# Optimization experiments

Hardware: AMD Instinct MI355X
Metric: run time of the kernel (lower is better)

The kernel has to match this reference:

```python
import jax, jax.numpy as jnp
import numpy as np

N_POINTS = 1 << 20
N_LEVELS = 16
F_PER_LVL = 2
LOG2_T = 19
T = 1 << LOG2_T
BASE_RES = 16
PER_LEVEL_SCALE = float(np.exp2(np.log2(2048.0 / 16.0) / (N_LEVELS - 1)))
# 8 trilinear corner offsets [8,3]
OFFSETS = np.stack(np.meshgrid(*([np.array([0, 1])] * 3), indexing='ij'), axis=-1).reshape(8, 3)
PRIMES = np.array([1, 2654435761, 805459861], dtype=np.uint32)  # tcnn spatial hash primes


def _level_params(l):
    # tcnn: grid_scale = 2^(l*log2(s)) * base - 1 ; resolution = ceil(scale)+1
    scale = np.exp2(l * np.log2(PER_LEVEL_SCALE)) * BASE_RES - 1.0
    res = int(np.ceil(scale)) + 1
    return float(scale), res


def hash_encode(x, table):
    """x: [N,3] in [0,1]; table: [L,T,F]. Returns [N, L*F]."""
    offs = jnp.asarray(OFFSETS)                     # [8,3] int32
    primes = jnp.asarray(PRIMES)                    # [3] uint32
    feats = []
    for l in range(N_LEVELS):
        scale, res = _level_params(l)
        pos = x * scale + 0.5                       # [N,3]
        pos_grid = jnp.floor(pos)
        w = pos - pos_grid                          # [N,3] interp weights
        c0 = pos_grid.astype(jnp.int32)             # [N,3]
        corners = c0[None, :, :] + offs[:, None, :]  # [8,N,3]
        if res ** 3 <= T:
            # dense indexing for coarse levels (fits in hashmap)
            cc = jnp.clip(corners, 0, res - 1)
            idx = cc[..., 0] + cc[..., 1] * res + cc[..., 2] * (res * res)
        else:
            cu = corners.astype(jnp.uint32)
            h = (cu[..., 0] * primes[0]) ^ (cu[..., 1] * primes[1]) ^ (cu[..., 2] * primes[2])
            idx = (h & jnp.uint32(T - 1)).astype(jnp.int32)
        f = table[l][idx]                           # [8,N,F] gather
        # trilinear weights: prod over dims of (w if corner bit else 1-w)
        wc = jnp.prod(jnp.where(offs[:, None, :] == 1, w[None], 1.0 - w[None]), axis=-1)  # [8,N]
        feats.append(jnp.sum(wc[..., None] * f, axis=0))  # [N,F]
    return jnp.concatenate(feats, axis=-1)          # [N, 32]


def _softplus10(z):
    return jax.nn.softplus(10.0 * z) / 10.0


def setup_inputs() -> dict:
    key = jax.random.key(0)
    k = jax.random.split(key, 6)
    x = jax.random.uniform(k[0], (N_POINTS, 3), dtype=jnp.float32)
    table = jax.random.normal(k[1], (N_LEVELS, T, F_PER_LVL), dtype=jnp.float32) * 1e-2
    w1 = jax.random.normal(k[2], (64, 32), dtype=jnp.float32) * 0.1
    w2 = jax.random.normal(k[3], (64, 64), dtype=jnp.float32) * 0.1
    w3 = jax.random.normal(k[4], (64, 64), dtype=jnp.float32) * 0.1
    w4 = jax.random.normal(k[5], (1, 64), dtype=jnp.float32) * 0.1
    return {"x": x, "table": table, "w1": w1, "w2": w2, "w3": w3, "w4": w4}


def reference(x, table, w1, w2, w3, w4):
    enc = hash_encode(x, table)                     # [N,32]
    h = _softplus10(enc @ w1.T)
    h = _softplus10(h @ w2.T)
    h = _softplus10(h @ w3.T)
    sdf = h @ w4.T                                  # [N,1]
    return sdf
```

## Files before the change

### kernel.cpp

```cpp
#include <hip/hip_runtime.h>
#include <cmath>

#define T_SIZE (1u << 19)

typedef _Float16 h8 __attribute__((ext_vector_type(8)));
typedef _Float16 h4 __attribute__((ext_vector_type(4)));
typedef _Float16 h2 __attribute__((ext_vector_type(2)));
typedef float f4 __attribute__((ext_vector_type(4)));

struct Levels {
    float scale[16];
    int   res[16];
    unsigned dense_mask;
};

__device__ __forceinline__ float softplus10(float z) {
    float e = __builtin_amdgcn_exp2f(fminf(z * 14.426950408889634f, 126.0f));
    return __builtin_amdgcn_logf(1.0f + e) * 0.069314718055994531f;
}

__global__ __launch_bounds__(256) void convert_table_kernel(
    const float2* __restrict__ t, h2* __restrict__ o, int total4)
{
    int i = blockIdx.x * 256 + threadIdx.x;
    if (i >= total4) return;
    const float2* src = t + (size_t)i * 4;
    h8 r;
#pragma unroll
    for (int j = 0; j < 4; ++j) {
        float2 v = src[j];
        r[2 * j]     = (_Float16)v.x;
        r[2 * j + 1] = (_Float16)v.y;
    }
    *(h8*)(o + (size_t)i * 4) = r;
}

__global__ __launch_bounds__(256) void convert_weights_kernel(
    const float* __restrict__ w1, const float* __restrict__ w2,
    const float* __restrict__ w3, _Float16* __restrict__ o)
{
    int i = blockIdx.x * 256 + threadIdx.x;
    float v;
    if (i < 2048)      v = w1[i];
    else if (i < 6144) v = w2[i - 2048];
    else               v = w3[i - 6144];
    o[i] = (_Float16)v;
}

__device__ __forceinline__ void gather_pair(
    const h2* __restrict__ tl, unsigned i0, unsigned i1,
    float2& v0, float2& v1)
{
    unsigned g = i0 & ~3u;
    union { h8 v; uint4 u; } cv;
    cv.v = *(const h8*)(tl + g);
    unsigned p0 = i0 & 3u;
    unsigned a01 = (p0 & 1u) ? cv.u.y : cv.u.x;
    unsigned a23 = (p0 & 1u) ? cv.u.w : cv.u.z;
    unsigned e0  = (p0 & 2u) ? a23 : a01;
    unsigned e1;
    if ((i1 & ~3u) == g) {
        unsigned p1 = i1 & 3u;
        unsigned b01 = (p1 & 1u) ? cv.u.y : cv.u.x;
        unsigned b23 = (p1 & 1u) ? cv.u.w : cv.u.z;
        e1 = (p1 & 2u) ? b23 : b01;
    } else {
        e1 = *(const unsigned*)(tl + i1);
    }
    h2 c0 = __builtin_bit_cast(h2, e0);
    h2 c1 = __builtin_bit_cast(h2, e1);
    v0 = make_float2((float)c0[0], (float)c0[1]);
    v1 = make_float2((float)c1[0], (float)c1[1]);
}

__global__ __launch_bounds__(256) void encode_kernel(
    const float* __restrict__ xs, const h2* __restrict__ table,
    h2* __restrict__ enc2, Levels lv, int lbase, int N)
{
    __shared__ float sx[768];
    __shared__ float s_scale[16];
    __shared__ int   s_res[16];

    const int i0 = blockIdx.x * 256;
    for (int t = threadIdx.x; t < 768; t += 256) sx[t] = xs[(size_t)i0 * 3 + t];
    if (threadIdx.x < 16) {
        s_scale[threadIdx.x] = lv.scale[threadIdx.x];
        s_res[threadIdx.x]   = lv.res[threadIdx.x];
    }
    __syncthreads();

    const int l = lbase + blockIdx.y;
    const int i = i0 + threadIdx.x;
    if (i >= N) return;

    const float px = sx[threadIdx.x * 3 + 0];
    const float py = sx[threadIdx.x * 3 + 1];
    const float pz = sx[threadIdx.x * 3 + 2];
    const float s  = s_scale[l];
    const int  res = s_res[l];

    float fx = px * s + 0.5f, fy = py * s + 0.5f, fz = pz * s + 0.5f;
    float gx = floorf(fx), gy = floorf(fy), gz = floorf(fz);
    float wx = fx - gx, wy = fy - gy, wz = fz - gz;
    int cx = (int)gx, cy = (int)gy, cz = (int)gz;

    const h2* tl = table + (size_t)l * T_SIZE;
    float2 vx0[4], vx1[4];

    if ((lv.dense_mask >> l) & 1u) {
        int r1 = res - 1;
        int x0 = min(cx, r1), x1 = min(cx + 1, r1);
        int y0 = min(cy, r1), y1 = min(cy + 1, r1);
        int z0 = min(cz, r1), z1 = min(cz + 1, r1);
        int rr = res * res;
        int bases[4] = {y0 * res + z0 * rr, y0 * res + z1 * rr,
                        y1 * res + z0 * rr, y1 * res + z1 * rr};
#pragma unroll
        for (int j = 0; j < 4; ++j)
            gather_pair(tl, (unsigned)(x0 + bases[j]), (unsigned)(x1 + bases[j]),
                        vx0[j], vx1[j]);
    } else {
        unsigned hy0 = (unsigned)cy * 2654435761u, hy1 = (unsigned)(cy + 1) * 2654435761u;
        unsigned hz0 = (unsigned)cz * 805459861u,  hz1 = (unsigned)(cz + 1) * 805459861u;
        unsigned Y[4] = {hy0 ^ hz0, hy0 ^ hz1, hy1 ^ hz0, hy1 ^ hz1};
        const unsigned M = T_SIZE - 1;
#pragma unroll
        for (int j = 0; j < 4; ++j)
            gather_pair(tl, ((unsigned)cx ^ Y[j]) & M,
                        ((unsigned)(cx + 1) ^ Y[j]) & M, vx0[j], vx1[j]);
    }

    float wx0 = 1.f - wx, wy0 = 1.f - wy, wz0 = 1.f - wz;
    float wyz[4] = {wy0 * wz0, wy0 * wz, wy * wz0, wy * wz};
    float f0 = 0.f, f1 = 0.f;
#pragma unroll
    for (int j = 0; j < 4; ++j) {
        float w0 = wx0 * wyz[j], w1 = wx * wyz[j];
        f0 += w0 * vx0[j].x + w1 * vx1[j].x;
        f1 += w0 * vx0[j].y + w1 * vx1[j].y;
    }

    h2 r;
    r[0] = (_Float16)f0;
    r[1] = (_Float16)f1;
    enc2[(size_t)l * N + i] = r;
}

template <typename WT>
__device__ __forceinline__ h8 load_frag8(const WT* p) {
    if constexpr (sizeof(WT) == 2) {
        return *(const h8*)p;
    } else {
        h8 r;
#pragma unroll
        for (int j = 0; j < 8; ++j) r[j] = (_Float16)p[j];
        return r;
    }
}

template <typename WT>
__global__ __launch_bounds__(256, 3) void mlp_kernel(
    const h2* __restrict__ enc2,
    const WT* __restrict__ w1, const WT* __restrict__ w2,
    const WT* __restrict__ w3, const float* __restrict__ w4,
    float* __restrict__ out, int nTiles, int N)
{
    constexpr int AR = 72;
    __shared__ __align__(16) _Float16 sAct[256 * AR];

    const int tid = threadIdx.x;
    const int wave = tid >> 6;
    const int lane = tid & 63;
    const int lrow = lane & 15;
    const int quad = lane >> 4;
    const int waveRow = wave * 64;
    const f4 zero = {0.f, 0.f, 0.f, 0.f};

    h8 aW1[4];
#pragma unroll
    for (int tm = 0; tm < 4; ++tm)
        aW1[tm] = load_frag8(w1 + (tm * 16 + lrow) * 32 + quad * 8);
    h8 aW2[4][2], aW3[4][2];
#pragma unroll
    for (int tm = 0; tm < 4; ++tm)
#pragma unroll
        for (int km = 0; km < 2; ++km) {
            aW2[tm][km] = load_frag8(w2 + (tm * 16 + lrow) * 64 + km * 32 + quad * 8);
            aW3[tm][km] = load_frag8(w3 + (tm * 16 + lrow) * 64 + km * 32 + quad * 8);
        }
    float w4f[16];
#pragma unroll
    for (int tm = 0; tm < 4; ++tm)
#pragma unroll
        for (int r = 0; r < 4; ++r)
            w4f[tm * 4 + r] = w4[tm * 16 + quad * 4 + r];

    for (int tile = blockIdx.x; tile < nTiles; tile += gridDim.x) {
        const int blockPt = tile * 256;

#pragma unroll
        for (int t = 0; t < 4; ++t) {
            const int ptg = blockPt + waveRow + t * 16 + lrow;
            h8 b;
#pragma unroll
            for (int d = 0; d < 4; ++d) {
                h2 p = enc2[(size_t)(quad * 4 + d) * N + ptg];
                b[2 * d]     = p[0];
                b[2 * d + 1] = p[1];
            }
            const int arow = (waveRow + t * 16 + lrow) * AR;
#pragma unroll
            for (int tm = 0; tm < 4; ++tm) {
                f4 acc = __builtin_amdgcn_mfma_f32_16x16x32_f16(aW1[tm], b, zero, 0, 0, 0);
                h4 pk;
#pragma unroll
                for (int r = 0; r < 4; ++r) pk[r] = (_Float16)softplus10(acc[r]);
                *(h4*)&sAct[arow + tm * 16 + quad * 4] = pk;
            }
        }

#pragma unroll
        for (int t = 0; t < 4; ++t) {
            const int arow = (waveRow + t * 16 + lrow) * AR;
            h8 b0 = *(const h8*)&sAct[arow + quad * 8];
            h8 b1 = *(const h8*)&sAct[arow + 32 + quad * 8];
            f4 accs[4];
#pragma unroll
            for (int tm = 0; tm < 4; ++tm) {
                f4 acc = __builtin_amdgcn_mfma_f32_16x16x32_f16(aW2[tm][0], b0, zero, 0, 0, 0);
                acc     = __builtin_amdgcn_mfma_f32_16x16x32_f16(aW2[tm][1], b1, acc,  0, 0, 0);
                accs[tm] = acc;
            }
#pragma unroll
            for (int tm = 0; tm < 4; ++tm) {
                h4 pk;
#pragma unroll
                for (int r = 0; r < 4; ++r) pk[r] = (_Float16)softplus10(accs[tm][r]);
                *(h4*)&sAct[arow + tm * 16 + quad * 4] = pk;
            }
        }

#pragma unroll
        for (int t = 0; t < 4; ++t) {
            const int arow = (waveRow + t * 16 + lrow) * AR;
            h8 b0 = *(const h8*)&sAct[arow + quad * 8];
            h8 b1 = *(const h8*)&sAct[arow + 32 + quad * 8];
            float sum = 0.f;
#pragma unroll
            for (int tm = 0; tm < 4; ++tm) {
                f4 acc = __builtin_amdgcn_mfma_f32_16x16x32_f16(aW3[tm][0], b0, zero, 0, 0, 0);
                acc     = __builtin_amdgcn_mfma_f32_16x16x32_f16(aW3[tm][1], b1, acc,  0, 0, 0);
#pragma unroll
                for (int r = 0; r < 4; ++r)
                    sum += w4f[tm * 4 + r] * softplus10(acc[r]);
            }
            sum += __shfl_xor(sum, 16, 64);
            sum += __shfl_xor(sum, 32, 64);
            if (quad == 0)
                out[blockPt + waveRow + t * 16 + lrow] = sum;
        }
    }
}

__global__ __launch_bounds__(256) void encode_kernel_f32(
    const float* __restrict__ xs, const float2* __restrict__ table,
    h2* __restrict__ enc2, Levels lv, int N)
{
    const int i = blockIdx.x * 256 + threadIdx.x;
    const int l = blockIdx.y;
    if (i >= N) return;
    float px = xs[3 * i], py = xs[3 * i + 1], pz = xs[3 * i + 2];
    float s = lv.scale[l];
    int res = lv.res[l];
    float fx = px * s + 0.5f, fy = py * s + 0.5f, fz = pz * s + 0.5f;
    float gx = floorf(fx), gy = floorf(fy), gz = floorf(fz);
    float wx = fx - gx, wy = fy - gy, wz = fz - gz;
    int cx = (int)gx, cy = (int)gy, cz = (int)gz;
    unsigned idx[8];
    if ((lv.dense_mask >> l) & 1u) {
        int r1 = res - 1;
        int x0 = min(cx, r1), x1 = min(cx + 1, r1);
        int y0 = min(cy, r1), y1 = min(cy + 1, r1);
        int z0 = min(cz, r1), z1 = min(cz + 1, r1);
        int rr = res * res;
        idx[0] = x0 + y0 * res + z0 * rr; idx[1] = x0 + y0 * res + z1 * rr;
        idx[2] = x0 + y1 * res + z0 * rr; idx[3] = x0 + y1 * res + z1 * rr;
        idx[4] = x1 + y0 * res + z0 * rr; idx[5] = x1 + y0 * res + z1 * rr;
        idx[6] = x1 + y1 * res + z0 * rr; idx[7] = x1 + y1 * res + z1 * rr;
    } else {
        unsigned hx0 = (unsigned)cx, hx1 = (unsigned)(cx + 1);
        unsigned hy0 = (unsigned)cy * 2654435761u, hy1 = (unsigned)(cy + 1) * 2654435761u;
        unsigned hz0 = (unsigned)cz * 805459861u,  hz1 = (unsigned)(cz + 1) * 805459861u;
        idx[0] = (hx0^hy0^hz0) & (T_SIZE-1); idx[1] = (hx0^hy0^hz1) & (T_SIZE-1);
        idx[2] = (hx0^hy1^hz0) & (T_SIZE-1); idx[3] = (hx0^hy1^hz1) & (T_SIZE-1);
        idx[4] = (hx1^hy0^hz0) & (T_SIZE-1); idx[5] = (hx1^hy0^hz1) & (T_SIZE-1);
        idx[6] = (hx1^hy1^hz0) & (T_SIZE-1); idx[7] = (hx1^hy1^hz1) & (T_SIZE-1);
    }
    const float2* tl = table + (size_t)l * T_SIZE;
    float wx0 = 1.f - wx, wy0 = 1.f - wy, wz0 = 1.f - wz;
    float wcs[8] = {wx0*wy0*wz0, wx0*wy0*wz, wx0*wy*wz0, wx0*wy*wz,
                    wx*wy0*wz0,  wx*wy0*wz,  wx*wy*wz0,  wx*wy*wz};
    float f0 = 0.f, f1 = 0.f;
#pragma unroll
    for (int c = 0; c < 8; ++c) {
        float2 v = tl[idx[c]];
        f0 += wcs[c] * v.x; f1 += wcs[c] * v.y;
    }
    h2 r; r[0] = (_Float16)f0; r[1] = (_Float16)f1;
    enc2[(size_t)l * N + i] = r;
}

extern "C" void kernel_launch(void* const* d_in, const int* in_sizes, int n_in,
                              void* d_out, int out_size, void* d_ws, size_t ws_size,
                              hipStream_t stream) {
    const float* x     = (const float*)d_in[0];
    const float* table = (const float*)d_in[1];
    const float* w1    = (const float*)d_in[2];
    const float* w2    = (const float*)d_in[3];
    const float* w3    = (const float*)d_in[4];
    const float* w4    = (const float*)d_in[5];
    float* out = (float*)d_out;
    const int N = in_sizes[0] / 3;

    Levels lv;
    lv.dense_mask = 0;
    const double pls = exp2(log2(2048.0 / 16.0) / 15.0);
    const double lg  = log2(pls);
    for (int l = 0; l < 16; ++l) {
        double sc = exp2((double)l * lg) * 16.0 - 1.0;
        int res = (int)ceil(sc) + 1;
        lv.scale[l] = (float)sc;
        lv.res[l]   = res;
        if ((long long)res * res * res <= (long long)T_SIZE) lv.dense_mask |= (1u << l);
    }

    const size_t encBytes   = (size_t)16 * N * 4;
    const size_t tableBytes = (size_t)16 * T_SIZE * 4;
    const size_t whBytes    = 32768;
    h2* enc2 = (h2*)d_ws;

    const int ptBlocks = (N + 255) / 256;
    const int nTiles = N / 256;
    const int mlpBlocks = 768;

    if (ws_size >= encBytes + tableBytes + whBytes) {
        h2* table16 = (h2*)((char*)d_ws + encBytes);
        _Float16* wh = (_Float16*)((char*)d_ws + encBytes + tableBytes);
        const int total4 = 16 * T_SIZE / 4;
        hipLaunchKernelGGL(convert_table_kernel, dim3((total4 + 255) / 256), dim3(256), 0,
                           stream, (const float2*)table, table16, total4);
        hipLaunchKernelGGL(convert_weights_kernel, dim3(40), dim3(256), 0, stream,
                           w1, w2, w3, wh);
        for (int lbase = 0; lbase < 16; lbase += 4)
            hipLaunchKernelGGL(encode_kernel, dim3(ptBlocks, 4), dim3(256), 0, stream,
                               x, (const h2*)table16, enc2, lv, lbase, N);
        hipLaunchKernelGGL((mlp_kernel<_Float16>), dim3(mlpBlocks), dim3(256), 0, stream,
                           enc2, wh, wh + 2048, wh + 6144, w4, out, nTiles, N);
    } else {
        hipLaunchKernelGGL(encode_kernel_f32, dim3(ptBlocks, 16), dim3(256), 0, stream,
                           x, (const float2*)table, enc2, lv, N);
        hipLaunchKernelGGL((mlp_kernel<float>), dim3(mlpBlocks), dim3(256), 0, stream,
                           enc2, w1, w2, w3, w4, out, nTiles, N);
    }
}
```

Before: 455.2 us.

## Fuse coarse and last-level encoding into MLP kernel, merge conversion kernels

Levels 5-14 are encoded by a single launch that writes to the intermediate buffer. Levels 0-4 and 15 are now computed inside the MLP kernel, which runs one block per 256-point tile and stages encodings per wave in shared memory. The table and weight conversion kernels are merged into one launch, and w4 is held as fp16 fragments. This removes several launches and part of the encoding round-trip through global memory. In exchange, gather latency moves into the MLP kernel, which has no persistent loop and may see lower occupancy from the extra registers.

```diff
diff --git a/kernel.cpp b/kernel.cpp
--- a/kernel.cpp
+++ b/kernel.cpp
@@ -19,32 +19,29 @@
     return __builtin_amdgcn_logf(1.0f + e) * 0.069314718055994531f;
 }
 
-__global__ __launch_bounds__(256) void convert_table_kernel(
-    const float2* __restrict__ t, h2* __restrict__ o, int total4)
+__global__ __launch_bounds__(256) void convert_kernel(
+    const float2* __restrict__ t, h2* __restrict__ o, int total4,
+    const float* __restrict__ w1, const float* __restrict__ w2,
+    const float* __restrict__ w3, _Float16* __restrict__ wh)
 {
     int i = blockIdx.x * 256 + threadIdx.x;
-    if (i >= total4) return;
-    const float2* src = t + (size_t)i * 4;
-    h8 r;
-#pragma unroll
-    for (int j = 0; j < 4; ++j) {
-        float2 v = src[j];
-        r[2 * j]     = (_Float16)v.x;
-        r[2 * j + 1] = (_Float16)v.y;
-    }
-    *(h8*)(o + (size_t)i * 4) = r;
-}
-
-__global__ __launch_bounds__(256) void convert_weights_kernel(
-    const float* __restrict__ w1, const float* __restrict__ w2,
-    const float* __restrict__ w3, _Float16* __restrict__ o)
-{
-    int i = blockIdx.x * 256 + threadIdx.x;
-    float v;
-    if (i < 2048)      v = w1[i];
-    else if (i < 6144) v = w2[i - 2048];
-    else               v = w3[i - 6144];
-    o[i] = (_Float16)v;
+    if (i < total4) {
+        const float2* src = t + (size_t)i * 4;
+        h8 r;
+#pragma unroll
+        for (int j = 0; j < 4; ++j) {
+            float2 v = src[j];
+            r[2 * j]     = (_Float16)v.x;
+            r[2 * j + 1] = (_Float16)v.y;
+        }
+        *(h8*)(o + (size_t)i * 4) = r;
+    } else {
+        int k = i - total4;
+        if (k < 10240) {
+            float v = (k < 2048) ? w1[k] : (k < 6144) ? w2[k - 2048] : w3[k - 6144];
+            wh[k] = (_Float16)v;
+        }
+    }
 }
 
 __device__ __forceinline__ void gather_pair(
@@ -73,41 +70,17 @@
     v1 = make_float2((float)c1[0], (float)c1[1]);
 }
 
-__global__ __launch_bounds__(256) void encode_kernel(
-    const float* __restrict__ xs, const h2* __restrict__ table,
-    h2* __restrict__ enc2, Levels lv, int lbase, int N)
-{
-    __shared__ float sx[768];
-    __shared__ float s_scale[16];
-    __shared__ int   s_res[16];
-
-    const int i0 = blockIdx.x * 256;
-    for (int t = threadIdx.x; t < 768; t += 256) sx[t] = xs[(size_t)i0 * 3 + t];
-    if (threadIdx.x < 16) {
-        s_scale[threadIdx.x] = lv.scale[threadIdx.x];
-        s_res[threadIdx.x]   = lv.res[threadIdx.x];
-    }
-    __syncthreads();
-
-    const int l = lbase + blockIdx.y;
-    const int i = i0 + threadIdx.x;
-    if (i >= N) return;
-
-    const float px = sx[threadIdx.x * 3 + 0];
-    const float py = sx[threadIdx.x * 3 + 1];
-    const float pz = sx[threadIdx.x * 3 + 2];
-    const float s  = s_scale[l];
-    const int  res = s_res[l];
-
+__device__ __forceinline__ h2 encode_point(
+    float px, float py, float pz, float s, int res, bool dense,
+    const h2* __restrict__ tl)
+{
     float fx = px * s + 0.5f, fy = py * s + 0.5f, fz = pz * s + 0.5f;
     float gx = floorf(fx), gy = floorf(fy), gz = floorf(fz);
     float wx = fx - gx, wy = fy - gy, wz = fz - gz;
     int cx = (int)gx, cy = (int)gy, cz = (int)gz;
 
-    const h2* tl = table + (size_t)l * T_SIZE;
     float2 vx0[4], vx1[4];
-
-    if ((lv.dense_mask >> l) & 1u) {
+    if (dense) {
         int r1 = res - 1;
         int x0 = min(cx, r1), x1 = min(cx + 1, r1);
         int y0 = min(cy, r1), y1 = min(cy + 1, r1);
@@ -139,10 +112,25 @@
         f0 += w0 * vx0[j].x + w1 * vx1[j].x;
         f1 += w0 * vx0[j].y + w1 * vx1[j].y;
     }
-
-    h2 r;
-    r[0] = (_Float16)f0;
-    r[1] = (_Float16)f1;
+    h2 r; r[0] = (_Float16)f0; r[1] = (_Float16)f1;
+    return r;
+}
+
+__global__ __launch_bounds__(256) void encode_kernel(
+    const float* __restrict__ xs, const h2* __restrict__ table,
+    h2* __restrict__ enc2, Levels lv, int lbase, int N)
+{
+    __shared__ float sx[768];
+    const int i0 = blockIdx.x * 256;
+    for (int t = threadIdx.x; t < 768; t += 256) sx[t] = xs[(size_t)i0 * 3 + t];
+    __syncthreads();
+
+    const int l = lbase + blockIdx.y;
+    const int i = i0 + threadIdx.x;
+    if (i >= N) return;
+    h2 r = encode_point(sx[threadIdx.x * 3], sx[threadIdx.x * 3 + 1],
+                        sx[threadIdx.x * 3 + 2], lv.scale[l], lv.res[l],
+                        (lv.dense_mask >> l) & 1u, table + (size_t)l * T_SIZE);
     enc2[(size_t)l * N + i] = r;
 }
 
@@ -158,23 +146,56 @@
     }
 }
 
-template <typename WT>
-__global__ __launch_bounds__(256, 3) void mlp_kernel(
+template <typename WT, bool LOCAL>
+__global__ __launch_bounds__(256, 3) void fused_kernel(
+    const float* __restrict__ xs, const h2* __restrict__ table16,
     const h2* __restrict__ enc2,
     const WT* __restrict__ w1, const WT* __restrict__ w2,
     const WT* __restrict__ w3, const float* __restrict__ w4,
-    float* __restrict__ out, int nTiles, int N)
+    float* __restrict__ out, Levels lv, int N)
 {
     constexpr int AR = 72;
-    __shared__ __align__(16) _Float16 sAct[256 * AR];
-
-    const int tid = threadIdx.x;
+    __shared__ __align__(16) char smem[4 * 9216];
+    __shared__ float sx[768];
+
+    const int tid  = threadIdx.x;
     const int wave = tid >> 6;
     const int lane = tid & 63;
     const int lrow = lane & 15;
     const int quad = lane >> 4;
-    const int waveRow = wave * 64;
+    const int base = blockIdx.x * 256;
+    char* wmem = smem + wave * 9216;
     const f4 zero = {0.f, 0.f, 0.f, 0.f};
+
+    for (int t = tid; t < 768; t += 256) sx[t] = xs[(size_t)base * 3 + t];
+    __syncthreads();
+    const float px = sx[tid * 3], py = sx[tid * 3 + 1], pz = sx[tid * 3 + 2];
+    const int p = tid & 63;
+
+    if (LOCAL) {
+#pragma unroll
+        for (int l = 5; l < 15; ++l) {
+            h2 v = enc2[(size_t)l * N + base + tid];
+            *(h2*)(wmem + ((l >> 2) << 10) + (p << 4) + ((l & 3) << 2)) = v;
+        }
+        const int LMAP[6] = {0, 1, 2, 3, 4, 15};
+#pragma unroll 2
+        for (int s6 = 0; s6 < 6; ++s6) {
+            const int l = LMAP[s6];
+            h2 v = encode_point(px, py, pz, lv.scale[l], lv.res[l],
+                                (lv.dense_mask >> l) & 1u,
+                                table16 + (size_t)l * T_SIZE);
+            *(h2*)(wmem + ((l >> 2) << 10) + (p << 4) + ((l & 3) << 2)) = v;
+        }
+    } else {
+#pragma unroll
+        for (int l = 0; l < 16; ++l) {
+            h2 v = enc2[(size_t)l * N + base + tid];
+            *(h2*)(wmem + ((l >> 2) << 10) + (p << 4) + ((l & 3) << 2)) = v;
+        }
+    }
+
+    asm volatile("" ::: "memory");
 
     h8 aW1[4];
 #pragma unroll
@@ -188,77 +209,71 @@
             aW2[tm][km] = load_frag8(w2 + (tm * 16 + lrow) * 64 + km * 32 + quad * 8);
             aW3[tm][km] = load_frag8(w3 + (tm * 16 + lrow) * 64 + km * 32 + quad * 8);
         }
-    float w4f[16];
+    h4 w4q[4];
 #pragma unroll
     for (int tm = 0; tm < 4; ++tm)
 #pragma unroll
-        for (int r = 0; r < 4; ++r)
-            w4f[tm * 4 + r] = w4[tm * 16 + quad * 4 + r];
-
-    for (int tile = blockIdx.x; tile < nTiles; tile += gridDim.x) {
-        const int blockPt = tile * 256;
-
-#pragma unroll
-        for (int t = 0; t < 4; ++t) {
-            const int ptg = blockPt + waveRow + t * 16 + lrow;
-            h8 b;
-#pragma unroll
-            for (int d = 0; d < 4; ++d) {
-                h2 p = enc2[(size_t)(quad * 4 + d) * N + ptg];
-                b[2 * d]     = p[0];
-                b[2 * d + 1] = p[1];
-            }
-            const int arow = (waveRow + t * 16 + lrow) * AR;
-#pragma unroll
-            for (int tm = 0; tm < 4; ++tm) {
-                f4 acc = __builtin_amdgcn_mfma_f32_16x16x32_f16(aW1[tm], b, zero, 0, 0, 0);
-                h4 pk;
-#pragma unroll
-                for (int r = 0; r < 4; ++r) pk[r] = (_Float16)softplus10(acc[r]);
-                *(h4*)&sAct[arow + tm * 16 + quad * 4] = pk;
-            }
-        }
-
-#pragma unroll
-        for (int t = 0; t < 4; ++t) {
-            const int arow = (waveRow + t * 16 + lrow) * AR;
-            h8 b0 = *(const h8*)&sAct[arow + quad * 8];
-            h8 b1 = *(const h8*)&sAct[arow + 32 + quad * 8];
-            f4 accs[4];
-#pragma unroll
-            for (int tm = 0; tm < 4; ++tm) {
-                f4 acc = __builtin_amdgcn_mfma_f32_16x16x32_f16(aW2[tm][0], b0, zero, 0, 0, 0);
-                acc     = __builtin_amdgcn_mfma_f32_16x16x32_f16(aW2[tm][1], b1, acc,  0, 0, 0);
-                accs[tm] = acc;
-            }
-#pragma unroll
-            for (int tm = 0; tm < 4; ++tm) {
-                h4 pk;
-#pragma unroll
-                for (int r = 0; r < 4; ++r) pk[r] = (_Float16)softplus10(accs[tm][r]);
-                *(h4*)&sAct[arow + tm * 16 + quad * 4] = pk;
-            }
-        }
-
-#pragma unroll
-        for (int t = 0; t < 4; ++t) {
-            const int arow = (waveRow + t * 16 + lrow) * AR;
-            h8 b0 = *(const h8*)&sAct[arow + quad * 8];
-            h8 b1 = *(const h8*)&sAct[arow + 32 + quad * 8];
-            float sum = 0.f;
-#pragma unroll
-            for (int tm = 0; tm < 4; ++tm) {
-                f4 acc = __builtin_amdgcn_mfma_f32_16x16x32_f16(aW3[tm][0], b0, zero, 0, 0, 0);
-                acc     = __builtin_amdgcn_mfma_f32_16x16x32_f16(aW3[tm][1], b1, acc,  0, 0, 0);
-#pragma unroll
-                for (int r = 0; r < 4; ++r)
-                    sum += w4f[tm * 4 + r] * softplus10(acc[r]);
-            }
-            sum += __shfl_xor(sum, 16, 64);
-            sum += __shfl_xor(sum, 32, 64);
-            if (quad == 0)
-                out[blockPt + waveRow + t * 16 + lrow] = sum;
-        }
+        for (int r = 0; r < 4; ++r) w4q[tm][r] = (_Float16)w4[tm * 16 + quad * 4 + r];
+
+    h8 bin[4];
+#pragma unroll
+    for (int t = 0; t < 4; ++t)
+        bin[t] = *(const h8*)(wmem + (quad << 10) + ((t * 16 + lrow) << 4));
+
+    _Float16* wAct = (_Float16*)wmem;
+
+#pragma unroll
+    for (int t = 0; t < 4; ++t) {
+        const int arow = (t * 16 + lrow) * AR;
+#pragma unroll
+        for (int tm = 0; tm < 4; ++tm) {
+            f4 acc = __builtin_amdgcn_mfma_f32_16x16x32_f16(aW1[tm], bin[t], zero, 0, 0, 0);
+            h4 pk;
+#pragma unroll
+            for (int r = 0; r < 4; ++r) pk[r] = (_Float16)softplus10(acc[r]);
+            *(h4*)&wAct[arow + tm * 16 + quad * 4] = pk;
+        }
+    }
+
+#pragma unroll
+    for (int t = 0; t < 4; ++t) {
+        const int arow = (t * 16 + lrow) * AR;
+        h8 b0 = *(const h8*)&wAct[arow + quad * 8];
+        h8 b1 = *(const h8*)&wAct[arow + 32 + quad * 8];
+        f4 accs[4];
+#pragma unroll
+        for (int tm = 0; tm < 4; ++tm) {
+            f4 acc = __builtin_amdgcn_mfma_f32_16x16x32_f16(aW2[tm][0], b0, zero, 0, 0, 0);
+            acc     = __builtin_amdgcn_mfma_f32_16x16x32_f16(aW2[tm][1], b1, acc,  0, 0, 0);
+            accs[tm] = acc;
+        }
+#pragma unroll
+        for (int tm = 0; tm < 4; ++tm) {
+            h4 pk;
+#pragma unroll
+            for (int r = 0; r < 4; ++r) pk[r] = (_Float16)softplus10(accs[tm][r]);
+            *(h4*)&wAct[arow + tm * 16 + quad * 4] = pk;
+        }
+    }
+
+#pragma unroll
+    for (int t = 0; t < 4; ++t) {
+        const int arow = (t * 16 + lrow) * AR;
+        h8 b0 = *(const h8*)&wAct[arow + quad * 8];
+        h8 b1 = *(const h8*)&wAct[arow + 32 + quad * 8];
+        float sum = 0.f;
+#pragma unroll
+        for (int tm = 0; tm < 4; ++tm) {
+            f4 acc = __builtin_amdgcn_mfma_f32_16x16x32_f16(aW3[tm][0], b0, zero, 0, 0, 0);
+            acc     = __builtin_amdgcn_mfma_f32_16x16x32_f16(aW3[tm][1], b1, acc,  0, 0, 0);
+#pragma unroll
+            for (int r = 0; r < 4; ++r)
+                sum += (float)w4q[tm][r] * softplus10(acc[r]);
+        }
+        sum += __shfl_xor(sum, 16, 64);
+        sum += __shfl_xor(sum, 32, 64);
+        if (quad == 0)
+            out[base + wave * 64 + t * 16 + lrow] = sum;
     }
 }
 
@@ -340,26 +355,24 @@
     h2* enc2 = (h2*)d_ws;
 
     const int ptBlocks = (N + 255) / 256;
-    const int nTiles = N / 256;
-    const int mlpBlocks = 768;
 
     if (ws_size >= encBytes + tableBytes + whBytes) {
         h2* table16 = (h2*)((char*)d_ws + encBytes);
         _Float16* wh = (_Float16*)((char*)d_ws + encBytes + tableBytes);
         const int total4 = 16 * T_SIZE / 4;
-        hipLaunchKernelGGL(convert_table_kernel, dim3((total4 + 255) / 256), dim3(256), 0,
-                           stream, (const float2*)table, table16, total4);
-        hipLaunchKernelGGL(convert_weights_kernel, dim3(40), dim3(256), 0, stream,
-                           w1, w2, w3, wh);
-        for (int lbase = 0; lbase < 16; lbase += 4)
-            hipLaunchKernelGGL(encode_kernel, dim3(ptBlocks, 4), dim3(256), 0, stream,
-                               x, (const h2*)table16, enc2, lv, lbase, N);
-        hipLaunchKernelGGL((mlp_kernel<_Float16>), dim3(mlpBlocks), dim3(256), 0, stream,
-                           enc2, wh, wh + 2048, wh + 6144, w4, out, nTiles, N);
+        const int convBlocks = (total4 + 10240 + 255) / 256;
+        hipLaunchKernelGGL(convert_kernel, dim3(convBlocks), dim3(256), 0, stream,
+                           (const float2*)table, table16, total4, w1, w2, w3, wh);
+        hipLaunchKernelGGL(encode_kernel, dim3(ptBlocks, 10), dim3(256), 0, stream,
+                           x, (const h2*)table16, enc2, lv, 5, N);
+        hipLaunchKernelGGL((fused_kernel<_Float16, true>), dim3(ptBlocks), dim3(256),
+                           0, stream, x, (const h2*)table16, (const h2*)enc2,
+                           wh, wh + 2048, wh + 6144, w4, out, lv, N);
     } else {
         hipLaunchKernelGGL(encode_kernel_f32, dim3(ptBlocks, 16), dim3(256), 0, stream,
                            x, (const float2*)table, enc2, lv, N);
-        hipLaunchKernelGGL((mlp_kernel<float>), dim3(mlpBlocks), dim3(256), 0, stream,
-                           enc2, w1, w2, w3, w4, out, nTiles, N);
-    }
-}
+        hipLaunchKernelGGL((fused_kernel<float, false>), dim3(ptBlocks), dim3(256),
+                           0, stream, x, (const h2*)nullptr, (const h2*)enc2,
+                           w1, w2, w3, w4, out, lv, N);
+    }
+}
```

Result: faster. 429.9 us (-5.6%).
